# Performance work log

Hardware: AMD Instinct MI355X
Metric: run time of the kernel (lower is better)

Reference implementation:

```python
import jax, jax.numpy as jnp
import numpy as np

B, C2D, C3D, H, W, N = 4, 64, 64, 256, 256, 16384
NEG_SLOPE = 0.1


def _conv1x1_lrelu(x, w, b):
    # 1x1 conv (no norm) + leaky_relu(0.1), per Conv2dNormRelu defaults
    y = jnp.einsum('bchw,oc->bohw', x, w) + b[None, :, None, None]
    return jax.nn.leaky_relu(y, NEG_SLOPE)


def _batch_gather(feat, idx):
    # feat: [B, C, N], idx: [B, P] -> [B, C, P]
    return jnp.take_along_axis(feat, idx[:, None, :], axis=2)


def setup_inputs() -> dict:
    key = jax.random.key(0)
    ks = jax.random.split(key, 14)
    f = jax.random.normal
    s = 0.05
    return {
        'xy': jax.random.uniform(ks[0], (B, 2, N), jnp.float32) * jnp.float32(W),
        'feat_2d': f(ks[1], (B, C2D, H, W), jnp.float32),
        'feat_3d': f(ks[2], (B, C3D, N), jnp.float32),
        'last_flow_2d': f(ks[3], (B, 2, H, W), jnp.float32),
        'last_flow_3d_to_2d': f(ks[4], (B, 2, N), jnp.float32),
        'nn_proj': jax.random.randint(ks[5], (B, H, W, 1), 0, N, jnp.int32),
        'w1': f(ks[6], (C3D, C3D + 5), jnp.float32) * s,
        'b1': f(ks[7], (C3D,), jnp.float32) * s,
        'w2': f(ks[8], (C3D, C3D), jnp.float32) * s,
        'b2': f(ks[9], (C3D,), jnp.float32) * s,
        'w3': f(ks[10], (C3D, C3D), jnp.float32) * s,
        'b3': f(ks[11], (C3D,), jnp.float32) * s,
        'wf': f(ks[12], (C2D, C2D + C3D), jnp.float32) * s,
        'bf': f(ks[13], (C2D,), jnp.float32) * s,
    }


def reference(xy, feat_2d, feat_3d, last_flow_2d, last_flow_3d_to_2d, nn_proj,
              w1, b1, w2, b2, w3, b3, wf, bf):
    b, _, h, w = feat_2d.shape
    # concat per-point flow onto 3D features: [B, C3D+2, N]
    feat_3d_aug = jnp.concatenate([feat_3d, last_flow_3d_to_2d], axis=1)

    idx = nn_proj[..., 0].reshape(b, h * w)  # nearest-neighbor point per pixel
    gathered = _batch_gather(feat_3d_aug, idx).reshape(b, -1, h, w)  # [B, C3D+2, H, W]
    xy_proj = _batch_gather(xy, idx).reshape(b, 2, h, w)             # [B, 2, H, W]

    # pixel-coordinate mesh grid: channel 0 = x (width), channel 1 = y (height)
    gy, gx = jnp.meshgrid(jnp.arange(h, dtype=xy.dtype), jnp.arange(w, dtype=xy.dtype), indexing='ij')
    grid = jnp.stack([gx, gy], axis=0)[None]  # [1, 2, H, W]
    offset = xy_proj - grid                    # [B, 2, H, W]

    # correlation between gathered 3D feats and 2D feats (channel mean)
    corr = jnp.mean(gathered[:, :C2D] * feat_2d, axis=1, keepdims=True)  # [B, 1, H, W]

    # last 2 channels are the projected flow; subtract detached last_flow_2d
    flow_ch = gathered[:, -2:] - jax.lax.stop_gradient(last_flow_2d)
    x = jnp.concatenate([corr, offset, gathered[:, :-2], flow_ch], axis=1)  # [B, C3D+5, H, W]

    x = _conv1x1_lrelu(x, w1, b1)
    x = _conv1x1_lrelu(x, w2, b2)
    x = _conv1x1_lrelu(x, w3, b3)
    out = _conv1x1_lrelu(jnp.concatenate([x, feat_2d], axis=1), wf, bf)  # [B, C2D, H, W]
    return out
```

## Files before the change

kernel.cpp:

```cpp
#include <hip/hip_runtime.h>

#define BB 4
#define CH 64
#define HW 65536
#define NN 16384
#define NT 128
#define XPITCH 72
#define LPITCH 72
#define W1OFS 0
#define W2OFS 4096
#define W3OFS 8192
#define WFOFS 12288
#define FWS_BYTE 46080
#define PTAB_BYTE 49152
#define PT_ROW 160
#define WS_NEED ((size_t)PTAB_BYTE + (size_t)BB * NN * PT_ROW)

typedef __attribute__((ext_vector_type(8))) short short8;
typedef __attribute__((ext_vector_type(4))) float f32x4;

union frag_u { unsigned short u[8]; short8 v; };
union row_u  { uint4 q[4]; unsigned short u[32]; };
union half_u { uint4 q[2]; unsigned short u[16]; };

static __device__ __forceinline__ unsigned short f2bf(float x) {
    unsigned int u = __float_as_uint(x);
    return (unsigned short)((u + 0x7fffu + ((u >> 16) & 1u)) >> 16);
}
static __device__ __forceinline__ float bf2f(unsigned short h) {
    return __uint_as_float(((unsigned int)h) << 16);
}

__global__ __launch_bounds__(256) void prep_w(
    const float* __restrict__ w1, const float* __restrict__ b1,
    const float* __restrict__ w2, const float* __restrict__ b2,
    const float* __restrict__ w3, const float* __restrict__ b3,
    const float* __restrict__ wf, const float* __restrict__ bf,
    unsigned short* __restrict__ wpk, float* __restrict__ fws)
{
    const int t = threadIdx.x;
    const int blk = blockIdx.x;
    if (blk == 0) {
        for (int i = t; i < 64 * 64; i += 256) {
            const int m = i >> 6, k = i & 63;
            wpk[W1OFS + i] = f2bf(w1[m * 69 + 3 + k]);
        }
    } else if (blk == 1) {
        for (int i = t; i < 64 * 64; i += 256) wpk[W2OFS + i] = f2bf(w2[i]);
    } else if (blk == 2) {
        for (int i = t; i < 64 * 64; i += 256) wpk[W3OFS + i] = f2bf(w3[i]);
    } else if (blk == 3) {
        for (int i = t; i < 64 * 128; i += 256) wpk[WFOFS + i] = f2bf(wf[i]);
    } else if (t < 64) {
        fws[t]       = b1[t];
        fws[64 + t]  = b2[t];
        fws[128 + t] = b3[t];
        fws[192 + t] = bf[t];
        fws[256 + t] = w1[t * 69 + 1];
        fws[320 + t] = w1[t * 69 + 2];
        fws[384 + t] = w1[t * 69 + 0];
        fws[448 + t] = w1[t * 69 + 67];
        fws[512 + t] = w1[t * 69 + 68];
    }
}

__global__ __launch_bounds__(256) void prep_t(
    const float* __restrict__ xy, const float* __restrict__ f3d,
    const float* __restrict__ lf3d, char* __restrict__ pt)
{
    const int t = threadIdx.x;
    const int cq = t >> 6;
    const int l = t & 63;
    const int gn = blockIdx.x * 64 + l;
    const int b = blockIdx.y;
    half_u r;
#pragma unroll
    for (int i = 0; i < 16; i++)
        r.u[i] = f2bf(f3d[(size_t)(b * CH + cq * 16 + i) * NN + gn]);
    char* row = pt + ((size_t)b * NN + gn) * PT_ROW;
    uint4* rq = (uint4*)row;
    rq[2 * cq] = r.q[0];
    rq[2 * cq + 1] = r.q[1];
    if (cq == 0) {
        float4 e;
        e.x = xy[(size_t)(b * 2 + 0) * NN + gn];
        e.y = xy[(size_t)(b * 2 + 1) * NN + gn];
        e.z = lf3d[(size_t)(b * 2 + 0) * NN + gn];
        e.w = lf3d[(size_t)(b * 2 + 1) * NN + gn];
        *(float4*)(row + 144) = e;
    }
}

template<int KT, int KROW, bool LO>
static __device__ __forceinline__ void layer_mfma(
    const unsigned short* __restrict__ wrow,
    const unsigned short* Xh, const unsigned short* Xl,
    int w, int ln, int q, f32x4 acc[4][2])
{
#pragma unroll
    for (int kt = 0; kt < KT; kt++) {
        const int kcol = kt * 32 + q * 8;
        short8 A[4];
#pragma unroll
        for (int mi = 0; mi < 4; mi++)
            A[mi] = *(const short8*)(wrow + (mi * 16 + ln) * KROW + kcol);
#pragma unroll
        for (int ni = 0; ni < 2; ni++) {
            const int nr = 32 * w + ni * 16 + ln;
            short8 bh = *(const short8*)(Xh + nr * XPITCH + kcol);
            short8 bl = bh;
            if (LO) bl = *(const short8*)(Xl + nr * LPITCH + kcol);
#pragma unroll
            for (int mi = 0; mi < 4; mi++) {
                acc[mi][ni] = __builtin_amdgcn_mfma_f32_16x16x32_bf16(A[mi], bh, acc[mi][ni], 0, 0, 0);
                if (LO)
                    acc[mi][ni] = __builtin_amdgcn_mfma_f32_16x16x32_bf16(A[mi], bl, acc[mi][ni], 0, 0, 0);
            }
        }
    }
}

static __device__ __forceinline__ void zero_acc(f32x4 acc[4][2]) {
#pragma unroll
    for (int mi = 0; mi < 4; mi++)
#pragma unroll
        for (int ni = 0; ni < 2; ni++)
#pragma unroll
            for (int r = 0; r < 4; r++) acc[mi][ni][r] = 0.f;
}

static __device__ __forceinline__ void epi_x(
    f32x4 acc[4][2], const float* __restrict__ fws, int bofs, bool off_fix,
    const float* offsp, const float* auxp, unsigned short* Xh, unsigned short* Xl,
    int w, int ln, int q)
{
#pragma unroll
    for (int mi = 0; mi < 4; mi++) {
        const float4 bias = *(const float4*)(fws + bofs + mi * 16 + q * 4);
        float4 wox = bias, woy = bias, wco = bias, wfx = bias, wfy = bias;
        if (off_fix) {
            wox = *(const float4*)(fws + 256 + mi * 16 + q * 4);
            woy = *(const float4*)(fws + 320 + mi * 16 + q * 4);
            wco = *(const float4*)(fws + 384 + mi * 16 + q * 4);
            wfx = *(const float4*)(fws + 448 + mi * 16 + q * 4);
            wfy = *(const float4*)(fws + 512 + mi * 16 + q * 4);
        }
#pragma unroll
        for (int ni = 0; ni < 2; ni++) {
            const int nr = 32 * w + ni * 16 + ln;
            float ox = 0.f, oy = 0.f, co = 0.f, fx = 0.f, fy = 0.f;
            if (off_fix) {
                ox = offsp[nr]; oy = offsp[NT + nr];
                co = auxp[nr];  fx = auxp[NT + nr]; fy = auxp[2 * NT + nr];
            }
            unsigned int hh0 = 0, hh1 = 0, ll0 = 0, ll1 = 0;
#pragma unroll
            for (int r = 0; r < 4; r++) {
                float a = acc[mi][ni][r] + ((const float*)&bias)[r];
                if (off_fix) {
                    a += ((const float*)&wox)[r] * ox + ((const float*)&woy)[r] * oy;
                    a += ((const float*)&wco)[r] * co;
                    a += ((const float*)&wfx)[r] * fx + ((const float*)&wfy)[r] * fy;
                }
                a = fmaxf(a, 0.1f * a);
                const unsigned short hb = f2bf(a);
                const unsigned short lb = f2bf(a - bf2f(hb));
                if (r == 0) { hh0 = hb; ll0 = lb; }
                if (r == 1) { hh0 |= ((unsigned)hb) << 16; ll0 |= ((unsigned)lb) << 16; }
                if (r == 2) { hh1 = hb; ll1 = lb; }
                if (r == 3) { hh1 |= ((unsigned)hb) << 16; ll1 |= ((unsigned)lb) << 16; }
            }
            *(uint2*)&Xh[nr * XPITCH + mi * 16 + q * 4] = make_uint2(hh0, hh1);
            *(uint2*)&Xl[nr * LPITCH + mi * 16 + q * 4] = make_uint2(ll0, ll1);
        }
    }
}

__global__ __launch_bounds__(256, 4) void fuse(
    const float* __restrict__ feat2d, const float* __restrict__ lf2d,
    const int* __restrict__ nn,
    const unsigned short* __restrict__ wpk, const float* __restrict__ fws,
    const char* __restrict__ ptab,
    float* __restrict__ out)
{
    __shared__ unsigned short Xhi[NT * XPITCH];
    __shared__ unsigned short Xlo[NT * LPITCH];
    __shared__ float offsS[2 * NT];
    __shared__ float auxS[3 * NT];

    const int tid = threadIdx.x;
    const int w = tid >> 6, lane = tid & 63;
    const int q = lane >> 4, ln = lane & 15;
    const int b = blockIdx.y;
    const int p0 = blockIdx.x * NT;

    {
        const int cp = lane >> 5, j = lane & 31;
        const int n = 32 * w + j;
        const int p = p0 + n;
        const int idx = nn[(size_t)b * HW + p];
        const char* prow = ptab + ((size_t)b * NN + idx) * PT_ROW;
        row_u g;
#pragma unroll
        for (int k = 0; k < 4; k++) g.q[k] = ((const uint4*)prow)[cp * 4 + k];
        float ca = 0.f;
#pragma unroll
        for (int i = 0; i < 32; i++) {
            const int c = cp * 32 + i;
            ca += feat2d[(size_t)(b * CH + c) * HW + p] * bf2f(g.u[i]);
        }
        uint4* xp = (uint4*)&Xhi[n * XPITCH + cp * 32];
#pragma unroll
        for (int k = 0; k < 4; k++) xp[k] = g.q[k];
        ca += __shfl_xor(ca, 32);
        if (cp == 0) {
            const float4 e = *(const float4*)(prow + 144);
            offsS[n] = e.x - (float)(p & 255);
            offsS[NT + n] = e.y - (float)(p >> 8);
            auxS[n] = ca * (1.0f / 64.0f);
            auxS[NT + n] = e.z - lf2d[(size_t)(b * 2 + 0) * HW + p];
            auxS[2 * NT + n] = e.w - lf2d[(size_t)(b * 2 + 1) * HW + p];
        }
    }

    f32x4 acc[4][2];
    zero_acc(acc);
    layer_mfma<2, 64, false>(wpk + W1OFS, Xhi, Xlo, w, ln, q, acc);
    epi_x(acc, fws, 0, true, offsS, auxS, Xhi, Xlo, w, ln, q);
    zero_acc(acc);
    layer_mfma<2, 64, true>(wpk + W2OFS, Xhi, Xlo, w, ln, q, acc);
    epi_x(acc, fws, 64, false, offsS, auxS, Xhi, Xlo, w, ln, q);
    zero_acc(acc);
    layer_mfma<2, 64, true>(wpk + W3OFS, Xhi, Xlo, w, ln, q, acc);
    epi_x(acc, fws, 128, false, offsS, auxS, Xhi, Xlo, w, ln, q);
    zero_acc(acc);
    layer_mfma<2, 128, true>(wpk + WFOFS, Xhi, Xlo, w, ln, q, acc);
#pragma unroll
    for (int kt = 2; kt < 4; kt++) {
        const int kcol = kt * 32 + q * 8;
        short8 A[4];
#pragma unroll
        for (int mi = 0; mi < 4; mi++)
            A[mi] = *(const short8*)(wpk + WFOFS + (mi * 16 + ln) * 128 + kcol);
#pragma unroll
        for (int ni = 0; ni < 2; ni++) {
            frag_u fh;
#pragma unroll
            for (int j = 0; j < 8; j++) {
                const int c = (kt - 2) * 32 + q * 8 + j;
                const float v = feat2d[(size_t)(b * CH + c) * HW + p0 + 32 * w + ni * 16 + ln];
                fh.u[j] = f2bf(v);
            }
#pragma unroll
            for (int mi = 0; mi < 4; mi++)
                acc[mi][ni] = __builtin_amdgcn_mfma_f32_16x16x32_bf16(A[mi], fh.v, acc[mi][ni], 0, 0, 0);
        }
    }
#pragma unroll
    for (int mi = 0; mi < 4; mi++) {
        const float4 bias = *(const float4*)(fws + 192 + mi * 16 + q * 4);
#pragma unroll
        for (int ni = 0; ni < 2; ni++) {
#pragma unroll
            for (int r = 0; r < 4; r++) {
                float a = acc[mi][ni][r] + ((const float*)&bias)[r];
                a = fmaxf(a, 0.1f * a);
                const int m = mi * 16 + q * 4 + r;
                out[(size_t)(b * CH + m) * HW + p0 + 32 * w + ni * 16 + ln] = a;
            }
        }
    }
}

__global__ __launch_bounds__(256) void fuse_slow(
    const float* __restrict__ feat2d, const float* __restrict__ lf2d,
    const float* __restrict__ xy, const float* __restrict__ feat3d,
    const float* __restrict__ lf3d, const int* __restrict__ nn,
    const float* __restrict__ w1, const float* __restrict__ b1,
    const float* __restrict__ w2, const float* __restrict__ b2,
    const float* __restrict__ w3, const float* __restrict__ b3,
    const float* __restrict__ wf, const float* __restrict__ bfv,
    float* __restrict__ out)
{
    const int p = blockIdx.x * 256 + threadIdx.x;
    const int b = blockIdx.y;
    const int idx = nn[(size_t)b * HW + p];
    const float* f3 = feat3d + (size_t)b * CH * NN + idx;
    float g[CH];
#pragma unroll
    for (int c = 0; c < CH; c++) g[c] = f3[(size_t)c * NN];
    const float fl3x = lf3d[(size_t)(b * 2 + 0) * NN + idx];
    const float fl3y = lf3d[(size_t)(b * 2 + 1) * NN + idx];
    const float xyx = xy[(size_t)(b * 2 + 0) * NN + idx];
    const float xyy = xy[(size_t)(b * 2 + 1) * NN + idx];
    const float* f2p = feat2d + (size_t)b * CH * HW + p;
    float corr = 0.f;
#pragma unroll
    for (int c = 0; c < CH; c++) corr += f2p[(size_t)c * HW] * g[c];
    corr *= (1.f / 64.f);
    float xin[69];
    xin[0] = corr;
    xin[1] = xyx - (float)(p & 255);
    xin[2] = xyy - (float)(p >> 8);
#pragma unroll
    for (int c = 0; c < CH; c++) xin[3 + c] = g[c];
    xin[67] = fl3x - lf2d[(size_t)(b * 2 + 0) * HW + p];
    xin[68] = fl3y - lf2d[(size_t)(b * 2 + 1) * HW + p];
    float x1[64], x2[64], x3[64], accv[64];
#pragma unroll
    for (int o = 0; o < 64; o++) {
        float a = b1[o];
#pragma unroll
        for (int k = 0; k < 69; k++) a += w1[o * 69 + k] * xin[k];
        x1[o] = (a >= 0.f) ? a : 0.1f * a;
    }
#pragma unroll
    for (int o = 0; o < 64; o++) {
        float a = b2[o];
#pragma unroll
        for (int k = 0; k < 64; k++) a += w2[o * 64 + k] * x1[k];
        x2[o] = (a >= 0.f) ? a : 0.1f * a;
    }
#pragma unroll
    for (int o = 0; o < 64; o++) {
        float a = b3[o];
#pragma unroll
        for (int k = 0; k < 64; k++) a += w3[o * 64 + k] * x2[k];
        x3[o] = (a >= 0.f) ? a : 0.1f * a;
    }
#pragma unroll
    for (int o = 0; o < 64; o++) {
        float a = bfv[o];
#pragma unroll
        for (int k = 0; k < 64; k++) a += wf[o * 128 + k] * x3[k];
        accv[o] = a;
    }
#pragma unroll
    for (int k = 0; k < 64; k++) {
        const float f = f2p[(size_t)k * HW];
#pragma unroll
        for (int o = 0; o < 64; o++) accv[o] += wf[o * 128 + 64 + k] * f;
    }
#pragma unroll
    for (int o = 0; o < 64; o++) {
        float a = accv[o];
        a = (a >= 0.f) ? a : 0.1f * a;
        out[(size_t)(b * CH + o) * HW + p] = a;
    }
}

extern "C" void kernel_launch(void* const* d_in, const int* in_sizes, int n_in,
                              void* d_out, int out_size, void* d_ws, size_t ws_size,
                              hipStream_t stream)
{
    const float* xy   = (const float*)d_in[0];
    const float* f2d  = (const float*)d_in[1];
    const float* f3d  = (const float*)d_in[2];
    const float* lf2d = (const float*)d_in[3];
    const float* lf3d = (const float*)d_in[4];
    const int*   nn   = (const int*)d_in[5];
    const float* w1 = (const float*)d_in[6];
    const float* b1 = (const float*)d_in[7];
    const float* w2 = (const float*)d_in[8];
    const float* b2 = (const float*)d_in[9];
    const float* w3 = (const float*)d_in[10];
    const float* b3 = (const float*)d_in[11];
    const float* wf = (const float*)d_in[12];
    const float* bf = (const float*)d_in[13];

    if (ws_size >= WS_NEED) {
        unsigned short* wpk = (unsigned short*)d_ws;
        float* fws = (float*)((char*)d_ws + FWS_BYTE);
        char* pt = (char*)d_ws + PTAB_BYTE;
        prep_w<<<dim3(5), 256, 0, stream>>>(w1, b1, w2, b2, w3, b3, wf, bf, wpk, fws);
        prep_t<<<dim3(NN / 64, BB), 256, 0, stream>>>(xy, f3d, lf3d, pt);
        fuse<<<dim3(HW / NT, BB), 256, 0, stream>>>(f2d, lf2d, nn, wpk, fws, pt, (float*)d_out);
    } else {
        fuse_slow<<<dim3(HW / 256, BB), 256, 0, stream>>>(f2d, lf2d, xy, f3d, lf3d, nn,
                                                          w1, b1, w2, b2, w3, b3, wf, bf,
                                                          (float*)d_out);
    }
}
```

Baseline: 227.1 us.

## Stage feat_2d tile in LDS as bf16 once, merge prep kernels

Loads the feat_2d tile once with float4 vector loads, converts it to bf16 and keeps it in a new shared buffer. Both the correlation dot product and the final layer's feat_2d operand now read from that buffer instead of issuing scalar global loads twice. The two prep kernels are merged into a single launch to save launch overhead. Min occupancy in launch bounds drops from 4 to 2 because of the added LDS. The correlation now uses bf16-rounded feat_2d, which lowers its precision.

```diff
diff --git a/kernel.cpp b/kernel.cpp
--- a/kernel.cpp
+++ b/kernel.cpp
@@ -7,6 +7,7 @@
 #define NT 128
 #define XPITCH 72
 #define LPITCH 72
+#define F2PITCH 72
 #define W1OFS 0
 #define W2OFS 4096
 #define W3OFS 8192
@@ -31,47 +32,48 @@
     return __uint_as_float(((unsigned int)h) << 16);
 }
 
-__global__ __launch_bounds__(256) void prep_w(
+__global__ __launch_bounds__(256) void prep(
+    const float* __restrict__ xy, const float* __restrict__ f3d,
+    const float* __restrict__ lf3d,
     const float* __restrict__ w1, const float* __restrict__ b1,
     const float* __restrict__ w2, const float* __restrict__ b2,
     const float* __restrict__ w3, const float* __restrict__ b3,
     const float* __restrict__ wf, const float* __restrict__ bf,
-    unsigned short* __restrict__ wpk, float* __restrict__ fws)
+    unsigned short* __restrict__ wpk, float* __restrict__ fws,
+    char* __restrict__ pt)
 {
     const int t = threadIdx.x;
-    const int blk = blockIdx.x;
-    if (blk == 0) {
-        for (int i = t; i < 64 * 64; i += 256) {
-            const int m = i >> 6, k = i & 63;
-            wpk[W1OFS + i] = f2bf(w1[m * 69 + 3 + k]);
-        }
-    } else if (blk == 1) {
-        for (int i = t; i < 64 * 64; i += 256) wpk[W2OFS + i] = f2bf(w2[i]);
-    } else if (blk == 2) {
-        for (int i = t; i < 64 * 64; i += 256) wpk[W3OFS + i] = f2bf(w3[i]);
-    } else if (blk == 3) {
-        for (int i = t; i < 64 * 128; i += 256) wpk[WFOFS + i] = f2bf(wf[i]);
-    } else if (t < 64) {
-        fws[t]       = b1[t];
-        fws[64 + t]  = b2[t];
-        fws[128 + t] = b3[t];
-        fws[192 + t] = bf[t];
-        fws[256 + t] = w1[t * 69 + 1];
-        fws[320 + t] = w1[t * 69 + 2];
-        fws[384 + t] = w1[t * 69 + 0];
-        fws[448 + t] = w1[t * 69 + 67];
-        fws[512 + t] = w1[t * 69 + 68];
-    }
-}
-
-__global__ __launch_bounds__(256) void prep_t(
-    const float* __restrict__ xy, const float* __restrict__ f3d,
-    const float* __restrict__ lf3d, char* __restrict__ pt)
-{
-    const int t = threadIdx.x;
+    const int bx = blockIdx.x;
+    if (bx >= NN / 64) {
+        if (blockIdx.y != 0) return;
+        const int blk = bx - NN / 64;
+        if (blk == 0) {
+            for (int i = t; i < 64 * 64; i += 256) {
+                const int m = i >> 6, k = i & 63;
+                wpk[W1OFS + i] = f2bf(w1[m * 69 + 3 + k]);
+            }
+        } else if (blk == 1) {
+            for (int i = t; i < 64 * 64; i += 256) wpk[W2OFS + i] = f2bf(w2[i]);
+        } else if (blk == 2) {
+            for (int i = t; i < 64 * 64; i += 256) wpk[W3OFS + i] = f2bf(w3[i]);
+        } else if (blk == 3) {
+            for (int i = t; i < 64 * 128; i += 256) wpk[WFOFS + i] = f2bf(wf[i]);
+        } else if (t < 64) {
+            fws[t]       = b1[t];
+            fws[64 + t]  = b2[t];
+            fws[128 + t] = b3[t];
+            fws[192 + t] = bf[t];
+            fws[256 + t] = w1[t * 69 + 1];
+            fws[320 + t] = w1[t * 69 + 2];
+            fws[384 + t] = w1[t * 69 + 0];
+            fws[448 + t] = w1[t * 69 + 67];
+            fws[512 + t] = w1[t * 69 + 68];
+        }
+        return;
+    }
     const int cq = t >> 6;
     const int l = t & 63;
-    const int gn = blockIdx.x * 64 + l;
+    const int gn = bx * 64 + l;
     const int b = blockIdx.y;
     half_u r;
 #pragma unroll
@@ -176,7 +178,7 @@
     }
 }
 
-__global__ __launch_bounds__(256, 4) void fuse(
+__global__ __launch_bounds__(256, 2) void fuse(
     const float* __restrict__ feat2d, const float* __restrict__ lf2d,
     const int* __restrict__ nn,
     const unsigned short* __restrict__ wpk, const float* __restrict__ fws,
@@ -185,6 +187,7 @@
 {
     __shared__ unsigned short Xhi[NT * XPITCH];
     __shared__ unsigned short Xlo[NT * LPITCH];
+    __shared__ unsigned short F2[NT * F2PITCH];
     __shared__ float offsS[2 * NT];
     __shared__ float auxS[3 * NT];
 
@@ -193,6 +196,26 @@
     const int q = lane >> 4, ln = lane & 15;
     const int b = blockIdx.y;
     const int p0 = blockIdx.x * NT;
+
+    {
+        const int ci = lane >> 3;
+        const int qd = lane & 7;
+        const int px0 = 32 * w + qd * 4;
+        float4 fv[8];
+#pragma unroll
+        for (int cc = 0; cc < 8; cc++) {
+            const int c = ci * 8 + cc;
+            fv[cc] = *(const float4*)(feat2d + (size_t)(b * CH + c) * HW + p0 + px0);
+        }
+#pragma unroll
+        for (int px = 0; px < 4; px++) {
+            frag_u fr;
+#pragma unroll
+            for (int cc = 0; cc < 8; cc++)
+                fr.u[cc] = f2bf(((const float*)&fv[cc])[px]);
+            *(short8*)&F2[(px0 + px) * F2PITCH + ci * 8] = fr.v;
+        }
+    }
 
     {
         const int cp = lane >> 5, j = lane & 31;
@@ -203,15 +226,17 @@
         row_u g;
 #pragma unroll
         for (int k = 0; k < 4; k++) g.q[k] = ((const uint4*)prow)[cp * 4 + k];
+        uint4* xp = (uint4*)&Xhi[n * XPITCH + cp * 32];
+#pragma unroll
+        for (int k = 0; k < 4; k++) xp[k] = g.q[k];
+        frag_u f2v[4];
+#pragma unroll
+        for (int k = 0; k < 4; k++)
+            f2v[k].v = *(const short8*)&F2[n * F2PITCH + cp * 32 + k * 8];
         float ca = 0.f;
 #pragma unroll
-        for (int i = 0; i < 32; i++) {
-            const int c = cp * 32 + i;
-            ca += feat2d[(size_t)(b * CH + c) * HW + p] * bf2f(g.u[i]);
-        }
-        uint4* xp = (uint4*)&Xhi[n * XPITCH + cp * 32];
-#pragma unroll
-        for (int k = 0; k < 4; k++) xp[k] = g.q[k];
+        for (int i = 0; i < 32; i++)
+            ca += bf2f(f2v[i >> 3].u[i & 7]) * bf2f(g.u[i]);
         ca += __shfl_xor(ca, 32);
         if (cp == 0) {
             const float4 e = *(const float4*)(prow + 144);
@@ -244,13 +269,9 @@
             A[mi] = *(const short8*)(wpk + WFOFS + (mi * 16 + ln) * 128 + kcol);
 #pragma unroll
         for (int ni = 0; ni < 2; ni++) {
+            const int nr = 32 * w + ni * 16 + ln;
             frag_u fh;
-#pragma unroll
-            for (int j = 0; j < 8; j++) {
-                const int c = (kt - 2) * 32 + q * 8 + j;
-                const float v = feat2d[(size_t)(b * CH + c) * HW + p0 + 32 * w + ni * 16 + ln];
-                fh.u[j] = f2bf(v);
-            }
+            fh.v = *(const short8*)&F2[nr * F2PITCH + (kt - 2) * 32 + q * 8];
 #pragma unroll
             for (int mi = 0; mi < 4; mi++)
                 acc[mi][ni] = __builtin_amdgcn_mfma_f32_16x16x32_bf16(A[mi], fh.v, acc[mi][ni], 0, 0, 0);
@@ -372,8 +393,9 @@
         unsigned short* wpk = (unsigned short*)d_ws;
         float* fws = (float*)((char*)d_ws + FWS_BYTE);
         char* pt = (char*)d_ws + PTAB_BYTE;
-        prep_w<<<dim3(5), 256, 0, stream>>>(w1, b1, w2, b2, w3, b3, wf, bf, wpk, fws);
-        prep_t<<<dim3(NN / 64, BB), 256, 0, stream>>>(xy, f3d, lf3d, pt);
+        prep<<<dim3(NN / 64 + 5, BB), 256, 0, stream>>>(xy, f3d, lf3d,
+                                                        w1, b1, w2, b2, w3, b3, wf, bf,
+                                                        wpk, fws, pt);
         fuse<<<dim3(HW / NT, BB), 256, 0, stream>>>(f2d, lf2d, nn, wpk, fws, pt, (float*)d_out);
     } else {
         fuse_slow<<<dim3(HW / 256, BB), 256, 0, stream>>>(f2d, lf2d, xy, f3d, lf3d, nn,
```

Result: faster. 219.9 us (-3.2%).
